# Kernel optimization log

Hardware: AMD Instinct MI355X
Metric: run time of the kernel (lower is better)

## Reference

```python
import jax, jax.numpy as jnp
import numpy as np
from jax.ops import segment_sum

N_NODES = 100000
IN_C, HID_C, OUT_C = 128, 128, 64
N_EDGES = 1600000


def gcn_conv(x, row, col, dinv, W, b):
    # PyG GCNConv: symmetric normalization with self-loops.
    # h = X W; out[c] = sum_{(r,c) in E} dinv[r]*dinv[c]*h[r] + dinv[v]^2*h[v] + b
    h = x @ W  # [N, F_out]
    norm = dinv[row] * dinv[col]  # [E]
    agg = segment_sum(h[row] * norm[:, None], col, num_segments=x.shape[0])
    agg = agg + h * (dinv * dinv)[:, None]  # self-loop contribution
    return agg + b


def setup_inputs() -> dict:
    key = jax.random.key(0)
    k1, k2, k3, k4, k5, k6 = jax.random.split(key, 6)
    x = jax.random.normal(k1, (N_NODES, IN_C), dtype=jnp.float32)
    edge_index = jax.random.randint(k2, (2, N_EDGES), 0, N_NODES, dtype=jnp.int64)
    # Glorot-style init for GCN weights, zero bias (as in PyG GCNConv)
    W1 = jax.random.normal(k3, (IN_C, HID_C), dtype=jnp.float32) / np.sqrt(IN_C)
    b1 = jnp.zeros((HID_C,), dtype=jnp.float32)
    W2 = jax.random.normal(k4, (HID_C, OUT_C), dtype=jnp.float32) / np.sqrt(HID_C)
    b2 = jnp.zeros((OUT_C,), dtype=jnp.float32)
    return {"x": x, "edge_index": edge_index, "W1": W1, "b1": b1, "W2": W2, "b2": b2}


def reference(x, edge_index, W1, b1, W2, b2):
    row, col = edge_index[0], edge_index[1]
    n = x.shape[0]
    # degree counts include self-loop (+1)
    deg = segment_sum(jnp.ones_like(col, dtype=x.dtype), col, num_segments=n) + 1.0
    dinv = jax.lax.rsqrt(deg)
    h = gcn_conv(x, row, col, dinv, W1, b1)
    h = jax.nn.relu(h)
    # dropout is identity in eval mode (get_embedding runs model.eval())
    out = gcn_conv(h, row, col, dinv, W2, b2)
    return out
```

## Files before the change

kernel.cpp:

```cpp
#include <hip/hip_runtime.h>
#include <math.h>


#define BS 256
#define EPB 4096
#define BK_SHIFT 9

typedef __attribute__((ext_vector_type(8))) short bf16x8;
typedef __attribute__((ext_vector_type(4))) float f32x4;
typedef __attribute__((ext_vector_type(4))) unsigned u32x4;

union FragU {
    bf16x8 v;
    unsigned u[4];
};

__device__ __forceinline__ unsigned pack_bf16x2(float a, float b) {
    unsigned ua = __float_as_uint(a);
    unsigned ub = __float_as_uint(b);
    ua = (ua + 0x7fffu + ((ua >> 16) & 1u)) >> 16;
    ub = (ub + 0x7fffu + ((ub >> 16) & 1u)) >> 16;
    return ua | (ub << 16);
}

__device__ __forceinline__ ushort bf16_rte(float a) {
    unsigned ua = __float_as_uint(a);
    return (ushort)((ua + 0x7fffu + ((ua >> 16) & 1u)) >> 16);
}

__device__ __forceinline__ float bf_lo(unsigned u) { return __uint_as_float(u << 16); }
__device__ __forceinline__ float bf_hi(unsigned u) { return __uint_as_float(u & 0xffff0000u); }

__global__ __launch_bounds__(BS) void p1_hist_kernel(const int* __restrict__ col,
                                                     int* __restrict__ countsT,
                                                     int E, int NBUCK, int NBLK) {
    __shared__ int h[256];
    int tid = threadIdx.x;
    h[tid] = 0;
    __syncthreads();
    int e0 = blockIdx.x * EPB;
    int e1 = min(e0 + EPB, E);
    for (int i = e0 + tid; i < e1; i += BS) atomicAdd(&h[col[i] >> BK_SHIFT], 1);
    __syncthreads();
    for (int b = tid; b < NBUCK; b += BS) countsT[b * NBLK + blockIdx.x] = h[b];
}

__global__ __launch_bounds__(BS) void scan_block_kernel(const int* __restrict__ in,
                                                        int* __restrict__ exc,
                                                        int* __restrict__ bsum, int N) {
    __shared__ int s[BS];
    int tid = threadIdx.x;
    int i = blockIdx.x * BS + tid;
    int v = (i < N) ? in[i] : 0;
    s[tid] = v;
    __syncthreads();
    for (int off = 1; off < BS; off <<= 1) {
        int t = (tid >= off) ? s[tid - off] : 0;
        __syncthreads();
        s[tid] += t;
        __syncthreads();
    }
    if (i < N) exc[i] = s[tid] - v;
    if (tid == BS - 1) bsum[blockIdx.x] = s[BS - 1];
}

__global__ __launch_bounds__(512) void scan_bsum_kernel(const int* __restrict__ bsum,
                                                        int* __restrict__ boff, int NB) {
    __shared__ int s[512];
    int tid = threadIdx.x;
    int v = (tid < NB) ? bsum[tid] : 0;
    s[tid] = v;
    __syncthreads();
    for (int off = 1; off < 512; off <<= 1) {
        int t = (tid >= off) ? s[tid - off] : 0;
        __syncthreads();
        s[tid] += t;
        __syncthreads();
    }
    if (tid < NB) boff[tid] = s[tid] - v;
}

__global__ __launch_bounds__(BS) void p2_scatter_kernel(const int* __restrict__ row,
                                                        const int* __restrict__ col,
                                                        const int* __restrict__ baseT,
                                                        const int* __restrict__ boff,
                                                        uint2* __restrict__ pairs,
                                                        int E, int NBUCK, int NBLK) {
    __shared__ int cur[256];
    int tid = threadIdx.x;
    for (int b = tid; b < NBUCK; b += BS) {
        int idx = b * NBLK + blockIdx.x;
        cur[b] = baseT[idx] + boff[idx >> 8];
    }
    __syncthreads();
    int e0 = blockIdx.x * EPB;
    int e1 = min(e0 + EPB, E);
    for (int i = e0 + tid; i < e1; i += BS) {
        int c = col[i];
        int r = row[i];
        int pos = atomicAdd(&cur[c >> BK_SHIFT], 1);
        pairs[pos] = make_uint2((unsigned)r, (unsigned)c);
    }
}

__global__ __launch_bounds__(BS) void p3_build_kernel(const uint2* __restrict__ pairs,
                                                      const int* __restrict__ baseT,
                                                      const int* __restrict__ boff,
                                                      int* __restrict__ off_g,
                                                      int* __restrict__ deg_g,
                                                      float* __restrict__ dinv,
                                                      int* __restrict__ src,
                                                      int E, int n, int NBUCK, int NBLK) {
    __shared__ int cnt[512];
    __shared__ int scn[512];
    __shared__ int a256[256];
    int tid = threadIdx.x;
    int b = blockIdx.x;
    int i0 = b * NBLK;
    int s = baseT[i0] + boff[i0 >> 8];
    int eEnd;
    if (b == NBUCK - 1) {
        eEnd = E;
    } else {
        int i1 = (b + 1) * NBLK;
        eEnd = baseT[i1] + boff[i1 >> 8];
    }

    cnt[tid] = 0;
    cnt[tid + 256] = 0;
    __syncthreads();
    for (int i = s + tid; i < eEnd; i += BS) {
        uint2 p = pairs[i];
        atomicAdd(&cnt[p.y & 511], 1);
    }
    __syncthreads();
    int pairsum = cnt[2 * tid] + cnt[2 * tid + 1];
    a256[tid] = pairsum;
    __syncthreads();
    for (int off = 1; off < 256; off <<= 1) {
        int t = (tid >= off) ? a256[tid - off] : 0;
        __syncthreads();
        a256[tid] += t;
        __syncthreads();
    }
    int exc = a256[tid] - pairsum;
    scn[2 * tid] = exc;
    scn[2 * tid + 1] = exc + cnt[2 * tid];
    __syncthreads();
#pragma unroll
    for (int l = tid; l < 512; l += BS) {
        int node = (b << BK_SHIFT) + l;
        if (node < n) {
            off_g[node] = s + scn[l];
            deg_g[node] = cnt[l];
            dinv[node] = rsqrtf((float)(cnt[l] + 1));
        }
    }
    __syncthreads();
#pragma unroll
    for (int l = tid; l < 512; l += BS) scn[l] += s;
    __syncthreads();
    for (int i = s + tid; i < eEnd; i += BS) {
        uint2 p = pairs[i];
        int pos = atomicAdd(&scn[p.y & 511], 1);
        src[pos] = (int)p.x;
    }
}

__global__ __launch_bounds__(BS) void wprep_kernel(const float* __restrict__ W1,
                                                   const float* __restrict__ W2,
                                                   ushort* __restrict__ wt1,
                                                   ushort* __restrict__ wt2) {
    int t = blockIdx.x * BS + threadIdx.x;
    if (t < 128 * 128) {
        int nn = t >> 7, k = t & 127;
        wt1[t] = bf16_rte(W1[k * 128 + nn]);
    }
    if (t < 64 * 128) {
        int nn = t >> 7, k = t & 127;
        wt2[t] = bf16_rte(W2[k * 64 + nn]);
    }
}

template <int NCH, bool IN_BF16>
__global__ __launch_bounds__(BS) void gemm_mfma_kernel(const void* __restrict__ Ain,
                                                       const ushort* __restrict__ WT,
                                                       const float* __restrict__ dinv,
                                                       unsigned* __restrict__ G, int n) {
    constexpr int NT = NCH / 16;
    constexpr int KP = 136;
    __shared__ ushort wlds[NCH * KP];

    int tid = threadIdx.x;
    for (int c = tid; c < NCH * 16; c += BS) {
        int nr = c >> 4, q16 = c & 15;
        *(uint4*)(wlds + nr * KP + q16 * 8) = ((const uint4*)WT)[c];
    }
    __syncthreads();

    int lane = tid & 63, wv = tid >> 6;
    int ml = lane & 15, quad = lane >> 4;
    int m = blockIdx.x * 64 + wv * 16 + ml;

    FragU b[4];
    if (m < n) {
        if (IN_BF16) {
#pragma unroll
            for (int ks = 0; ks < 4; ++ks) {
                uint4 t = ((const uint4*)Ain)[(size_t)m * 16 + ks * 4 + quad];
                b[ks].u[0] = t.x; b[ks].u[1] = t.y; b[ks].u[2] = t.z; b[ks].u[3] = t.w;
            }
        } else {
            const float4* A = (const float4*)Ain + (size_t)m * 32;
#pragma unroll
            for (int ks = 0; ks < 4; ++ks) {
                float4 p0 = A[ks * 8 + quad * 2];
                float4 p1 = A[ks * 8 + quad * 2 + 1];
                b[ks].u[0] = pack_bf16x2(p0.x, p0.y);
                b[ks].u[1] = pack_bf16x2(p0.z, p0.w);
                b[ks].u[2] = pack_bf16x2(p1.x, p1.y);
                b[ks].u[3] = pack_bf16x2(p1.z, p1.w);
            }
        }
    } else {
#pragma unroll
        for (int ks = 0; ks < 4; ++ks) {
            b[ks].u[0] = 0; b[ks].u[1] = 0; b[ks].u[2] = 0; b[ks].u[3] = 0;
        }
    }

    f32x4 acc[NT];
#pragma unroll
    for (int nt = 0; nt < NT; ++nt) {
        acc[nt][0] = 0.f; acc[nt][1] = 0.f; acc[nt][2] = 0.f; acc[nt][3] = 0.f;
    }

#pragma unroll
    for (int nt = 0; nt < NT; ++nt) {
#pragma unroll
        for (int ks = 0; ks < 4; ++ks) {
            bf16x8 a = *(const bf16x8*)(wlds + (nt * 16 + ml) * KP + ks * 32 + quad * 8);
            acc[nt] = __builtin_amdgcn_mfma_f32_16x16x32_bf16(a, b[ks].v, acc[nt], 0, 0, 0);
        }
    }

    if (m < n) {
        float dv = dinv[m];
        unsigned* grow = G + (size_t)m * (NCH / 2);
#pragma unroll
        for (int nt = 0; nt < NT; ++nt) {
            uint2 o;
            o.x = pack_bf16x2(acc[nt][0] * dv, acc[nt][1] * dv);
            o.y = pack_bf16x2(acc[nt][2] * dv, acc[nt][3] * dv);
            *(uint2*)(grow + nt * 8 + quad * 2) = o;
        }
    }
}

template <int C, bool RELU, bool OUT_BF16>
__global__ __launch_bounds__(BS) void agg_kernel(const unsigned* __restrict__ G,
                                                 const int* __restrict__ edge_off,
                                                 const int* __restrict__ cnt,
                                                 const int* __restrict__ src,
                                                 const float* __restrict__ dinv,
                                                 const float* __restrict__ bias,
                                                 void* __restrict__ out, int n) {
    constexpr int Gp = C / 8;
    constexpr int NPB = BS / Gp;
    int lane = threadIdx.x & (Gp - 1);
    int li = threadIdx.x / Gp;
    int node = blockIdx.x * NPB + li;
    if (node >= n) return;

    const uint4* G4 = (const uint4*)G;
    float acc[8];
    {
        uint4 sv = G4[(size_t)node * Gp + lane];
        acc[0] = bf_lo(sv.x); acc[1] = bf_hi(sv.x);
        acc[2] = bf_lo(sv.y); acc[3] = bf_hi(sv.y);
        acc[4] = bf_lo(sv.z); acc[5] = bf_hi(sv.z);
        acc[6] = bf_lo(sv.w); acc[7] = bf_hi(sv.w);
    }
    const int* sp = src + edge_off[node];
    int deg = cnt[node];

#define ACCUM(v)                                                               \
    acc[0] += bf_lo(v.x); acc[1] += bf_hi(v.x);                                \
    acc[2] += bf_lo(v.y); acc[3] += bf_hi(v.y);                                \
    acc[4] += bf_lo(v.z); acc[5] += bf_hi(v.z);                                \
    acc[6] += bf_lo(v.w); acc[7] += bf_hi(v.w);

    if constexpr (Gp == 16) {
        int i = 0;
        for (; i + Gp <= deg; i += Gp) {
            int myi = __builtin_nontemporal_load(sp + i + lane);
#pragma unroll
            for (int h = 0; h < Gp / 8; ++h) {
                uint4 v[8];
#pragma unroll
                for (int u = 0; u < 8; ++u) {
                    int s = __shfl(myi, h * 8 + u, Gp);
                    v[u] = G4[(size_t)s * Gp + lane];
                }
#pragma unroll
                for (int u = 0; u < 8; ++u) { ACCUM(v[u]) }
            }
        }
        int rem = deg - i;
        if (rem > 0) {
            int myi = (lane < rem) ? __builtin_nontemporal_load(sp + i + lane) : 0;
            int j = 0;
            if (rem >= 8) {
                uint4 v[8];
#pragma unroll
                for (int u = 0; u < 8; ++u) {
                    int s = __shfl(myi, u, Gp);
                    v[u] = G4[(size_t)s * Gp + lane];
                }
#pragma unroll
                for (int u = 0; u < 8; ++u) { ACCUM(v[u]) }
                j = 8;
            }
            if (rem - j >= 4) {
                uint4 v[4];
#pragma unroll
                for (int u = 0; u < 4; ++u) {
                    int s = __shfl(myi, j + u, Gp);
                    v[u] = G4[(size_t)s * Gp + lane];
                }
#pragma unroll
                for (int u = 0; u < 4; ++u) { ACCUM(v[u]) }
                j += 4;
            }
            if (rem - j >= 2) {
                int s0 = __shfl(myi, j, Gp);
                int s1 = __shfl(myi, j + 1, Gp);
                uint4 v0 = G4[(size_t)s0 * Gp + lane];
                uint4 v1 = G4[(size_t)s1 * Gp + lane];
                ACCUM(v0) ACCUM(v1)
                j += 2;
            }
            if (rem - j >= 1) {
                int s0 = __shfl(myi, j, Gp);
                uint4 v0 = G4[(size_t)s0 * Gp + lane];
                ACCUM(v0)
            }
        }
    } else {
        int myi0 = __builtin_nontemporal_load(sp + lane);
        int myi1 = __builtin_nontemporal_load(sp + 8 + lane);
        int i = 0;
        for (; i + 16 <= deg; i += 16) {
            int nx0 = __builtin_nontemporal_load(sp + i + 16 + lane);
            int nx1 = __builtin_nontemporal_load(sp + i + 24 + lane);
            uint4 v[8];
#pragma unroll
            for (int u = 0; u < 8; ++u) {
                int s = __shfl(myi0, u, Gp);
                v[u] = G4[(size_t)s * Gp + lane];
            }
#pragma unroll
            for (int u = 0; u < 8; ++u) { ACCUM(v[u]) }
#pragma unroll
            for (int u = 0; u < 8; ++u) {
                int s = __shfl(myi1, u, Gp);
                v[u] = G4[(size_t)s * Gp + lane];
            }
#pragma unroll
            for (int u = 0; u < 8; ++u) { ACCUM(v[u]) }
            myi0 = nx0;
            myi1 = nx1;
        }
        int rem = deg - i;
        if (rem >= 8) {
            uint4 v[8];
#pragma unroll
            for (int u = 0; u < 8; ++u) {
                int s = __shfl(myi0, u, Gp);
                v[u] = G4[(size_t)s * Gp + lane];
            }
#pragma unroll
            for (int u = 0; u < 8; ++u) { ACCUM(v[u]) }
        }
        int rest = (rem >= 8) ? myi1 : myi0;
        int jb = 0;
        int r2 = rem & 7;
        if (r2 >= 4) {
            uint4 v[4];
#pragma unroll
            for (int u = 0; u < 4; ++u) {
                int s = __shfl(rest, jb + u, Gp);
                v[u] = G4[(size_t)s * Gp + lane];
            }
#pragma unroll
            for (int u = 0; u < 4; ++u) { ACCUM(v[u]) }
            jb += 4;
        }
        if (r2 & 2) {
            int s0 = __shfl(rest, jb, Gp);
            int s1 = __shfl(rest, jb + 1, Gp);
            uint4 v0 = G4[(size_t)s0 * Gp + lane];
            uint4 v1 = G4[(size_t)s1 * Gp + lane];
            ACCUM(v0) ACCUM(v1)
            jb += 2;
        }
        if (r2 & 1) {
            int s0 = __shfl(rest, jb, Gp);
            uint4 v0 = G4[(size_t)s0 * Gp + lane];
            ACCUM(v0)
        }
    }
#undef ACCUM

    float dv = dinv[node];
    const float4* b4 = (const float4*)bias;
    float4 bl = b4[2 * lane + 0], bh = b4[2 * lane + 1];
    float o0x = acc[0] * dv + bl.x, o0y = acc[1] * dv + bl.y;
    float o0z = acc[2] * dv + bl.z, o0w = acc[3] * dv + bl.w;
    float o1x = acc[4] * dv + bh.x, o1y = acc[5] * dv + bh.y;
    float o1z = acc[6] * dv + bh.z, o1w = acc[7] * dv + bh.w;
    if (RELU) {
        o0x = fmaxf(o0x, 0.f); o0y = fmaxf(o0y, 0.f);
        o0z = fmaxf(o0z, 0.f); o0w = fmaxf(o0w, 0.f);
        o1x = fmaxf(o1x, 0.f); o1y = fmaxf(o1y, 0.f);
        o1z = fmaxf(o1z, 0.f); o1w = fmaxf(o1w, 0.f);
    }
    if (OUT_BF16) {
        u32x4 ov;
        ov.x = pack_bf16x2(o0x, o0y);
        ov.y = pack_bf16x2(o0z, o0w);
        ov.z = pack_bf16x2(o1x, o1y);
        ov.w = pack_bf16x2(o1z, o1w);
        __builtin_nontemporal_store(ov, (u32x4*)out + (size_t)node * Gp + lane);
    } else {
        f32x4* orow = (f32x4*)((float*)out + (size_t)node * C);
        f32x4 o0; o0.x = o0x; o0.y = o0y; o0.z = o0z; o0.w = o0w;
        f32x4 o1; o1.x = o1x; o1.y = o1y; o1.z = o1z; o1.w = o1w;
        __builtin_nontemporal_store(o0, orow + 2 * lane + 0);
        __builtin_nontemporal_store(o1, orow + 2 * lane + 1);
    }
}

extern "C" void kernel_launch(void* const* d_in, const int* in_sizes, int n_in,
                              void* d_out, int out_size, void* d_ws, size_t ws_size,
                              hipStream_t stream) {
    const float* x  = (const float*)d_in[0];
    const int*   ei = (const int*)d_in[1];
    const float* W1 = (const float*)d_in[2];
    const float* b1 = (const float*)d_in[3];
    const float* W2 = (const float*)d_in[4];
    const float* b2 = (const float*)d_in[5];

    const int IN_C = 128, HID_C = 128;
    int n = in_sizes[0] / IN_C;
    int E = in_sizes[1] / 2;
    const int* row = ei;
    const int* col = ei + E;

    int NBUCK = (n + 511) >> BK_SHIFT;
    int NBLK = (E + EPB - 1) / EPB;
    int M = NBUCK * NBLK;
    int NBS = (M + BS - 1) / BS;

    char* w = (char*)d_ws;
    auto alloc = [&](size_t bytes) {
        void* p = (void*)w;
        w += (bytes + 255) & ~(size_t)255;
        return p;
    };
    int*      countsT = (int*)alloc((size_t)M * 4);
    int*      baseT   = (int*)alloc((size_t)M * 4);
    int*      bsum    = (int*)alloc((size_t)NBS * 4);
    int*      boff    = (int*)alloc((size_t)NBS * 4);
    uint2*    pairs   = (uint2*)alloc((size_t)E * 8);
    int*      src     = (int*)alloc((size_t)E * 4);
    int*      off     = (int*)alloc((size_t)n * 4);
    int*      deg     = (int*)alloc((size_t)n * 4);
    float*    dinv    = (float*)alloc((size_t)n * 4);
    ushort*   wt1     = (ushort*)alloc(128 * 128 * 2);
    ushort*   wt2     = (ushort*)alloc(64 * 128 * 2);
    unsigned* g       = (unsigned*)alloc((size_t)n * HID_C * 2);
    unsigned* h1b     = (unsigned*)alloc((size_t)n * HID_C * 2);

    wprep_kernel<<<64, BS, 0, stream>>>(W1, W2, wt1, wt2);

    p1_hist_kernel<<<NBLK, BS, 0, stream>>>(col, countsT, E, NBUCK, NBLK);
    scan_block_kernel<<<NBS, BS, 0, stream>>>(countsT, baseT, bsum, M);
    scan_bsum_kernel<<<1, 512, 0, stream>>>(bsum, boff, NBS);
    p2_scatter_kernel<<<NBLK, BS, 0, stream>>>(row, col, baseT, boff, pairs,
                                               E, NBUCK, NBLK);
    p3_build_kernel<<<NBUCK, BS, 0, stream>>>(pairs, baseT, boff, off, deg, dinv,
                                              src, E, n, NBUCK, NBLK);

    int gridM = (n + 63) / 64;

    gemm_mfma_kernel<128, false><<<gridM, BS, 0, stream>>>(x, wt1, dinv, g, n);
    agg_kernel<128, true, true><<<(n + 15) / 16, BS, 0, stream>>>(g, off, deg, src,
                                                                  dinv, b1, h1b, n);

    gemm_mfma_kernel<64, true><<<gridM, BS, 0, stream>>>(h1b, wt2, dinv, g, n);
    agg_kernel<64, false, false><<<(n + 31) / 32, BS, 0, stream>>>(g, off, deg, src,
                                                                   dinv, b2, d_out, n);
}
```

Before: 276.7 us.

## Replace two-pass bucket sort CSR build with global atomic counting sort

Replaces the bucketed histogram, scatter-to-pairs and per-bucket local sort with a direct counting sort: global atomic degree counts, a prefix scan over nodes, and a placement pass using global atomics on per-node cursors. This drops the intermediate pairs buffer and one extra pass over all edges. In exchange it relies on contended global atomics with random addresses and writes src in scattered order. Edge order within a node becomes nondeterministic, which can change float summation order.

```diff
diff --git a/kernel.cpp b/kernel.cpp
--- a/kernel.cpp
+++ b/kernel.cpp
@@ -3,8 +3,6 @@
 
 
 #define BS 256
-#define EPB 4096
-#define BK_SHIFT 9
 
 typedef __attribute__((ext_vector_type(8))) short bf16x8;
 typedef __attribute__((ext_vector_type(4))) float f32x4;
@@ -31,18 +29,38 @@
 __device__ __forceinline__ float bf_lo(unsigned u) { return __uint_as_float(u << 16); }
 __device__ __forceinline__ float bf_hi(unsigned u) { return __uint_as_float(u & 0xffff0000u); }
 
-__global__ __launch_bounds__(BS) void p1_hist_kernel(const int* __restrict__ col,
-                                                     int* __restrict__ countsT,
-                                                     int E, int NBUCK, int NBLK) {
-    __shared__ int h[256];
-    int tid = threadIdx.x;
-    h[tid] = 0;
-    __syncthreads();
-    int e0 = blockIdx.x * EPB;
-    int e1 = min(e0 + EPB, E);
-    for (int i = e0 + tid; i < e1; i += BS) atomicAdd(&h[col[i] >> BK_SHIFT], 1);
-    __syncthreads();
-    for (int b = tid; b < NBUCK; b += BS) countsT[b * NBLK + blockIdx.x] = h[b];
+__global__ __launch_bounds__(BS) void wprep_zero_kernel(const float* __restrict__ W1,
+                                                        const float* __restrict__ W2,
+                                                        ushort* __restrict__ wt1,
+                                                        ushort* __restrict__ wt2,
+                                                        int* __restrict__ deg, int n) {
+    int t = blockIdx.x * BS + threadIdx.x;
+    int NT = gridDim.x * BS;
+    for (int i = t; i < n; i += NT) deg[i] = 0;
+    if (t < 128 * 128) {
+        int nn = t >> 7, k = t & 127;
+        wt1[t] = bf16_rte(W1[k * 128 + nn]);
+    }
+    if (t < 64 * 128) {
+        int nn = t >> 7, k = t & 127;
+        wt2[t] = bf16_rte(W2[k * 64 + nn]);
+    }
+}
+
+__global__ __launch_bounds__(BS) void count_kernel(const int* __restrict__ col,
+                                                   int* __restrict__ deg, int E) {
+    int t = blockIdx.x * BS + threadIdx.x;
+    int n4 = E >> 2;
+    const int4* c4 = (const int4*)col;
+    if (t < n4) {
+        int4 c = c4[t];
+        atomicAdd(&deg[c.x], 1);
+        atomicAdd(&deg[c.y], 1);
+        atomicAdd(&deg[c.z], 1);
+        atomicAdd(&deg[c.w], 1);
+    }
+    int r = (n4 << 2) + t;
+    if (r < E) atomicAdd(&deg[col[r]], 1);
 }
 
 __global__ __launch_bounds__(BS) void scan_block_kernel(const int* __restrict__ in,
@@ -80,105 +98,45 @@
     if (tid < NB) boff[tid] = s[tid] - v;
 }
 
-__global__ __launch_bounds__(BS) void p2_scatter_kernel(const int* __restrict__ row,
-                                                        const int* __restrict__ col,
-                                                        const int* __restrict__ baseT,
-                                                        const int* __restrict__ boff,
-                                                        uint2* __restrict__ pairs,
-                                                        int E, int NBUCK, int NBLK) {
-    __shared__ int cur[256];
-    int tid = threadIdx.x;
-    for (int b = tid; b < NBUCK; b += BS) {
-        int idx = b * NBLK + blockIdx.x;
-        cur[b] = baseT[idx] + boff[idx >> 8];
-    }
-    __syncthreads();
-    int e0 = blockIdx.x * EPB;
-    int e1 = min(e0 + EPB, E);
-    for (int i = e0 + tid; i < e1; i += BS) {
-        int c = col[i];
-        int r = row[i];
-        int pos = atomicAdd(&cur[c >> BK_SHIFT], 1);
-        pairs[pos] = make_uint2((unsigned)r, (unsigned)c);
-    }
-}
-
-__global__ __launch_bounds__(BS) void p3_build_kernel(const uint2* __restrict__ pairs,
-                                                      const int* __restrict__ baseT,
-                                                      const int* __restrict__ boff,
-                                                      int* __restrict__ off_g,
-                                                      int* __restrict__ deg_g,
-                                                      float* __restrict__ dinv,
-                                                      int* __restrict__ src,
-                                                      int E, int n, int NBUCK, int NBLK) {
-    __shared__ int cnt[512];
-    __shared__ int scn[512];
-    __shared__ int a256[256];
-    int tid = threadIdx.x;
-    int b = blockIdx.x;
-    int i0 = b * NBLK;
-    int s = baseT[i0] + boff[i0 >> 8];
-    int eEnd;
-    if (b == NBUCK - 1) {
-        eEnd = E;
-    } else {
-        int i1 = (b + 1) * NBLK;
-        eEnd = baseT[i1] + boff[i1 >> 8];
-    }
-
-    cnt[tid] = 0;
-    cnt[tid + 256] = 0;
-    __syncthreads();
-    for (int i = s + tid; i < eEnd; i += BS) {
-        uint2 p = pairs[i];
-        atomicAdd(&cnt[p.y & 511], 1);
-    }
-    __syncthreads();
-    int pairsum = cnt[2 * tid] + cnt[2 * tid + 1];
-    a256[tid] = pairsum;
-    __syncthreads();
-    for (int off = 1; off < 256; off <<= 1) {
-        int t = (tid >= off) ? a256[tid - off] : 0;
-        __syncthreads();
-        a256[tid] += t;
-        __syncthreads();
-    }
-    int exc = a256[tid] - pairsum;
-    scn[2 * tid] = exc;
-    scn[2 * tid + 1] = exc + cnt[2 * tid];
-    __syncthreads();
-#pragma unroll
-    for (int l = tid; l < 512; l += BS) {
-        int node = (b << BK_SHIFT) + l;
-        if (node < n) {
-            off_g[node] = s + scn[l];
-            deg_g[node] = cnt[l];
-            dinv[node] = rsqrtf((float)(cnt[l] + 1));
-        }
-    }
-    __syncthreads();
-#pragma unroll
-    for (int l = tid; l < 512; l += BS) scn[l] += s;
-    __syncthreads();
-    for (int i = s + tid; i < eEnd; i += BS) {
-        uint2 p = pairs[i];
-        int pos = atomicAdd(&scn[p.y & 511], 1);
-        src[pos] = (int)p.x;
-    }
-}
-
-__global__ __launch_bounds__(BS) void wprep_kernel(const float* __restrict__ W1,
-                                                   const float* __restrict__ W2,
-                                                   ushort* __restrict__ wt1,
-                                                   ushort* __restrict__ wt2) {
+__global__ __launch_bounds__(BS) void init_kernel(const int* __restrict__ exc,
+                                                  const int* __restrict__ boff,
+                                                  const int* __restrict__ deg,
+                                                  int* __restrict__ off,
+                                                  int* __restrict__ cur,
+                                                  float* __restrict__ dinv, int n) {
+    int i = blockIdx.x * BS + threadIdx.x;
+    if (i < n) {
+        int base = exc[i] + boff[i >> 8];
+        off[i] = base;
+        cur[i] = base;
+        dinv[i] = rsqrtf((float)(deg[i] + 1));
+    }
+}
+
+__global__ __launch_bounds__(BS) void place_kernel(const int* __restrict__ row,
+                                                   const int* __restrict__ col,
+                                                   int* __restrict__ cur,
+                                                   int* __restrict__ src, int E) {
     int t = blockIdx.x * BS + threadIdx.x;
-    if (t < 128 * 128) {
-        int nn = t >> 7, k = t & 127;
-        wt1[t] = bf16_rte(W1[k * 128 + nn]);
-    }
-    if (t < 64 * 128) {
-        int nn = t >> 7, k = t & 127;
-        wt2[t] = bf16_rte(W2[k * 64 + nn]);
+    int n4 = E >> 2;
+    const int4* c4 = (const int4*)col;
+    const int4* r4 = (const int4*)row;
+    if (t < n4) {
+        int4 c = c4[t];
+        int4 r = r4[t];
+        int p0 = atomicAdd(&cur[c.x], 1);
+        int p1 = atomicAdd(&cur[c.y], 1);
+        int p2 = atomicAdd(&cur[c.z], 1);
+        int p3 = atomicAdd(&cur[c.w], 1);
+        src[p0] = r.x;
+        src[p1] = r.y;
+        src[p2] = r.z;
+        src[p3] = r.w;
+    }
+    int rr = (n4 << 2) + t;
+    if (rr < E) {
+        int p = atomicAdd(&cur[col[rr]], 1);
+        src[p] = row[rr];
     }
 }
 
@@ -457,10 +415,7 @@
     const int* row = ei;
     const int* col = ei + E;
 
-    int NBUCK = (n + 511) >> BK_SHIFT;
-    int NBLK = (E + EPB - 1) / EPB;
-    int M = NBUCK * NBLK;
-    int NBS = (M + BS - 1) / BS;
+    int NBS = (n + BS - 1) / BS;
 
     char* w = (char*)d_ws;
     auto alloc = [&](size_t bytes) {
@@ -468,29 +423,29 @@
         w += (bytes + 255) & ~(size_t)255;
         return p;
     };
-    int*      countsT = (int*)alloc((size_t)M * 4);
-    int*      baseT   = (int*)alloc((size_t)M * 4);
+    int*      deg     = (int*)alloc((size_t)n * 4);
+    int*      exc     = (int*)alloc((size_t)n * 4);
     int*      bsum    = (int*)alloc((size_t)NBS * 4);
     int*      boff    = (int*)alloc((size_t)NBS * 4);
-    uint2*    pairs   = (uint2*)alloc((size_t)E * 8);
+    int*      cur     = (int*)alloc((size_t)n * 4);
+    int*      off     = (int*)alloc((size_t)n * 4);
+    float*    dinv    = (float*)alloc((size_t)n * 4);
     int*      src     = (int*)alloc((size_t)E * 4);
-    int*      off     = (int*)alloc((size_t)n * 4);
-    int*      deg     = (int*)alloc((size_t)n * 4);
-    float*    dinv    = (float*)alloc((size_t)n * 4);
     ushort*   wt1     = (ushort*)alloc(128 * 128 * 2);
     ushort*   wt2     = (ushort*)alloc(64 * 128 * 2);
     unsigned* g       = (unsigned*)alloc((size_t)n * HID_C * 2);
     unsigned* h1b     = (unsigned*)alloc((size_t)n * HID_C * 2);
 
-    wprep_kernel<<<64, BS, 0, stream>>>(W1, W2, wt1, wt2);
-
-    p1_hist_kernel<<<NBLK, BS, 0, stream>>>(col, countsT, E, NBUCK, NBLK);
-    scan_block_kernel<<<NBS, BS, 0, stream>>>(countsT, baseT, bsum, M);
+    int n4 = E >> 2;
+    int gridE = (n4 + BS - 1) / BS;
+
+    wprep_zero_kernel<<<64, BS, 0, stream>>>(W1, W2, wt1, wt2, deg, n);
+
+    count_kernel<<<gridE, BS, 0, stream>>>(col, deg, E);
+    scan_block_kernel<<<NBS, BS, 0, stream>>>(deg, exc, bsum, n);
     scan_bsum_kernel<<<1, 512, 0, stream>>>(bsum, boff, NBS);
-    p2_scatter_kernel<<<NBLK, BS, 0, stream>>>(row, col, baseT, boff, pairs,
-                                               E, NBUCK, NBLK);
-    p3_build_kernel<<<NBUCK, BS, 0, stream>>>(pairs, baseT, boff, off, deg, dinv,
-                                              src, E, n, NBUCK, NBLK);
+    init_kernel<<<NBS, BS, 0, stream>>>(exc, boff, deg, off, cur, dinv, n);
+    place_kernel<<<gridE, BS, 0, stream>>>(row, col, cur, src, E);
 
     int gridM = (n + 63) / 64;
 
```

After: 412.0 us. +48.9%, slower.

## Fuse CSR build stages into one cooperative kernel with grid syncs

Applied to the files above, without the earlier changes.

Merges weight prep, histogram, two-level scan, scatter and per-bucket CSR build into a single cooperative launch of 256 blocks separated by grid.sync(), replacing six kernel launches. It also drops the edges-per-block count from 4096 (about 391 blocks) to 256 blocks of about 6250 edges each, which shrinks the count matrix. The goal is to remove launch gaps and tail effects between the small preprocessing kernels. In exchange, grid-wide barriers cost something, only 256 blocks run the edge passes, and the build phase still uses only NBUCK (about 196) blocks.

```diff
diff --git a/kernel.cpp b/kernel.cpp
--- a/kernel.cpp
+++ b/kernel.cpp
@@ -1,10 +1,13 @@
 #include <hip/hip_runtime.h>
+#include <hip/hip_cooperative_groups.h>
 #include <math.h>
 
 
 #define BS 256
-#define EPB 4096
 #define BK_SHIFT 9
+#define NG 256
+
+namespace cg = cooperative_groups;
 
 typedef __attribute__((ext_vector_type(8))) short bf16x8;
 typedef __attribute__((ext_vector_type(4))) float f32x4;
@@ -31,154 +34,140 @@
 __device__ __forceinline__ float bf_lo(unsigned u) { return __uint_as_float(u << 16); }
 __device__ __forceinline__ float bf_hi(unsigned u) { return __uint_as_float(u & 0xffff0000u); }
 
-__global__ __launch_bounds__(BS) void p1_hist_kernel(const int* __restrict__ col,
-                                                     int* __restrict__ countsT,
-                                                     int E, int NBUCK, int NBLK) {
-    __shared__ int h[256];
+__global__ __launch_bounds__(BS) void csr_fused_kernel(
+        const int* __restrict__ row, const int* __restrict__ col,
+        const float* __restrict__ W1, const float* __restrict__ W2,
+        ushort* __restrict__ wt1, ushort* __restrict__ wt2,
+        int* __restrict__ countsT, int* __restrict__ bsum,
+        int* __restrict__ boff, uint2* __restrict__ pairs,
+        int* __restrict__ off_g, int* __restrict__ deg_g,
+        float* __restrict__ dinv, int* __restrict__ src,
+        int E, int n, int NBUCK, int NSC) {
+    cg::grid_group grid = cg::this_grid();
+    __shared__ int s1[512];
+    __shared__ int s2[512];
+    __shared__ int s3[256];
+
     int tid = threadIdx.x;
-    h[tid] = 0;
+    int blk = blockIdx.x;
+    int gt = blk * BS + tid;
+    int M = NBUCK * NG;
+    int EPB = (E + NG - 1) / NG;
+    int e0 = blk * EPB;
+    int e1 = min(e0 + EPB, E);
+
+    if (gt < 128 * 128) {
+        int nn = gt >> 7, k = gt & 127;
+        wt1[gt] = bf16_rte(W1[k * 128 + nn]);
+    }
+    if (gt < 64 * 128) {
+        int nn = gt >> 7, k = gt & 127;
+        wt2[gt] = bf16_rte(W2[k * 64 + nn]);
+    }
+    s3[tid] = 0;
     __syncthreads();
-    int e0 = blockIdx.x * EPB;
-    int e1 = min(e0 + EPB, E);
-    for (int i = e0 + tid; i < e1; i += BS) atomicAdd(&h[col[i] >> BK_SHIFT], 1);
+    for (int i = e0 + tid; i < e1; i += BS) atomicAdd(&s3[col[i] >> BK_SHIFT], 1);
     __syncthreads();
-    for (int b = tid; b < NBUCK; b += BS) countsT[b * NBLK + blockIdx.x] = h[b];
-}
-
-__global__ __launch_bounds__(BS) void scan_block_kernel(const int* __restrict__ in,
-                                                        int* __restrict__ exc,
-                                                        int* __restrict__ bsum, int N) {
-    __shared__ int s[BS];
-    int tid = threadIdx.x;
-    int i = blockIdx.x * BS + tid;
-    int v = (i < N) ? in[i] : 0;
-    s[tid] = v;
+    for (int b = tid; b < NBUCK; b += BS) countsT[b * NG + blk] = s3[b];
+    grid.sync();
+
+    if (blk < NSC) {
+        int i = blk * BS + tid;
+        int v = (i < M) ? countsT[i] : 0;
+        s3[tid] = v;
+        __syncthreads();
+        for (int off = 1; off < BS; off <<= 1) {
+            int t = (tid >= off) ? s3[tid - off] : 0;
+            __syncthreads();
+            s3[tid] += t;
+            __syncthreads();
+        }
+        if (i < M) countsT[i] = s3[tid] - v;
+        if (tid == BS - 1) bsum[blk] = s3[BS - 1];
+    }
+    grid.sync();
+
+    if (blk == 0) {
+        int carry = 0;
+        for (int c0 = 0; c0 < NSC; c0 += BS) {
+            int idx = c0 + tid;
+            int v = (idx < NSC) ? bsum[idx] : 0;
+            s3[tid] = v;
+            __syncthreads();
+            for (int off = 1; off < BS; off <<= 1) {
+                int t = (tid >= off) ? s3[tid - off] : 0;
+                __syncthreads();
+                s3[tid] += t;
+                __syncthreads();
+            }
+            if (idx < NSC) boff[idx] = s3[tid] - v + carry;
+            int tot = s3[BS - 1];
+            __syncthreads();
+            carry += tot;
+        }
+    }
+    grid.sync();
+
+    if (blk < NSC) {
+        int i = blk * BS + tid;
+        if (i < M) countsT[i] += boff[blk];
+    }
+    grid.sync();
+
+    for (int b = tid; b < NBUCK; b += BS) s3[b] = countsT[b * NG + blk];
     __syncthreads();
-    for (int off = 1; off < BS; off <<= 1) {
-        int t = (tid >= off) ? s[tid - off] : 0;
-        __syncthreads();
-        s[tid] += t;
-        __syncthreads();
-    }
-    if (i < N) exc[i] = s[tid] - v;
-    if (tid == BS - 1) bsum[blockIdx.x] = s[BS - 1];
-}
-
-__global__ __launch_bounds__(512) void scan_bsum_kernel(const int* __restrict__ bsum,
-                                                        int* __restrict__ boff, int NB) {
-    __shared__ int s[512];
-    int tid = threadIdx.x;
-    int v = (tid < NB) ? bsum[tid] : 0;
-    s[tid] = v;
-    __syncthreads();
-    for (int off = 1; off < 512; off <<= 1) {
-        int t = (tid >= off) ? s[tid - off] : 0;
-        __syncthreads();
-        s[tid] += t;
-        __syncthreads();
-    }
-    if (tid < NB) boff[tid] = s[tid] - v;
-}
-
-__global__ __launch_bounds__(BS) void p2_scatter_kernel(const int* __restrict__ row,
-                                                        const int* __restrict__ col,
-                                                        const int* __restrict__ baseT,
-                                                        const int* __restrict__ boff,
-                                                        uint2* __restrict__ pairs,
-                                                        int E, int NBUCK, int NBLK) {
-    __shared__ int cur[256];
-    int tid = threadIdx.x;
-    for (int b = tid; b < NBUCK; b += BS) {
-        int idx = b * NBLK + blockIdx.x;
-        cur[b] = baseT[idx] + boff[idx >> 8];
-    }
-    __syncthreads();
-    int e0 = blockIdx.x * EPB;
-    int e1 = min(e0 + EPB, E);
     for (int i = e0 + tid; i < e1; i += BS) {
         int c = col[i];
         int r = row[i];
-        int pos = atomicAdd(&cur[c >> BK_SHIFT], 1);
+        int pos = atomicAdd(&s3[c >> BK_SHIFT], 1);
         pairs[pos] = make_uint2((unsigned)r, (unsigned)c);
     }
-}
-
-__global__ __launch_bounds__(BS) void p3_build_kernel(const uint2* __restrict__ pairs,
-                                                      const int* __restrict__ baseT,
-                                                      const int* __restrict__ boff,
-                                                      int* __restrict__ off_g,
-                                                      int* __restrict__ deg_g,
-                                                      float* __restrict__ dinv,
-                                                      int* __restrict__ src,
-                                                      int E, int n, int NBUCK, int NBLK) {
-    __shared__ int cnt[512];
-    __shared__ int scn[512];
-    __shared__ int a256[256];
-    int tid = threadIdx.x;
-    int b = blockIdx.x;
-    int i0 = b * NBLK;
-    int s = baseT[i0] + boff[i0 >> 8];
-    int eEnd;
-    if (b == NBUCK - 1) {
-        eEnd = E;
-    } else {
-        int i1 = (b + 1) * NBLK;
-        eEnd = baseT[i1] + boff[i1 >> 8];
-    }
-
-    cnt[tid] = 0;
-    cnt[tid + 256] = 0;
-    __syncthreads();
-    for (int i = s + tid; i < eEnd; i += BS) {
-        uint2 p = pairs[i];
-        atomicAdd(&cnt[p.y & 511], 1);
-    }
-    __syncthreads();
-    int pairsum = cnt[2 * tid] + cnt[2 * tid + 1];
-    a256[tid] = pairsum;
-    __syncthreads();
-    for (int off = 1; off < 256; off <<= 1) {
-        int t = (tid >= off) ? a256[tid - off] : 0;
-        __syncthreads();
-        a256[tid] += t;
-        __syncthreads();
-    }
-    int exc = a256[tid] - pairsum;
-    scn[2 * tid] = exc;
-    scn[2 * tid + 1] = exc + cnt[2 * tid];
-    __syncthreads();
-#pragma unroll
-    for (int l = tid; l < 512; l += BS) {
-        int node = (b << BK_SHIFT) + l;
-        if (node < n) {
-            off_g[node] = s + scn[l];
-            deg_g[node] = cnt[l];
-            dinv[node] = rsqrtf((float)(cnt[l] + 1));
-        }
-    }
-    __syncthreads();
-#pragma unroll
-    for (int l = tid; l < 512; l += BS) scn[l] += s;
-    __syncthreads();
-    for (int i = s + tid; i < eEnd; i += BS) {
-        uint2 p = pairs[i];
-        int pos = atomicAdd(&scn[p.y & 511], 1);
-        src[pos] = (int)p.x;
-    }
-}
-
-__global__ __launch_bounds__(BS) void wprep_kernel(const float* __restrict__ W1,
-                                                   const float* __restrict__ W2,
-                                                   ushort* __restrict__ wt1,
-                                                   ushort* __restrict__ wt2) {
-    int t = blockIdx.x * BS + threadIdx.x;
-    if (t < 128 * 128) {
-        int nn = t >> 7, k = t & 127;
-        wt1[t] = bf16_rte(W1[k * 128 + nn]);
-    }
-    if (t < 64 * 128) {
-        int nn = t >> 7, k = t & 127;
-        wt2[t] = bf16_rte(W2[k * 64 + nn]);
+    grid.sync();
+
+    if (blk < NBUCK) {
+        int b = blk;
+        int s = countsT[b * NG];
+        int eEnd = (b == NBUCK - 1) ? E : countsT[(b + 1) * NG];
+
+        s1[tid] = 0;
+        s1[tid + 256] = 0;
+        __syncthreads();
+        for (int i = s + tid; i < eEnd; i += BS) {
+            uint2 p = pairs[i];
+            atomicAdd(&s1[p.y & 511], 1);
+        }
+        __syncthreads();
+        int pairsum = s1[2 * tid] + s1[2 * tid + 1];
+        s3[tid] = pairsum;
+        __syncthreads();
+        for (int off = 1; off < 256; off <<= 1) {
+            int t = (tid >= off) ? s3[tid - off] : 0;
+            __syncthreads();
+            s3[tid] += t;
+            __syncthreads();
+        }
+        int exc = s3[tid] - pairsum;
+        s2[2 * tid] = exc;
+        s2[2 * tid + 1] = exc + s1[2 * tid];
+        __syncthreads();
+#pragma unroll
+        for (int l = tid; l < 512; l += BS) {
+            int node = (b << BK_SHIFT) + l;
+            if (node < n) {
+                off_g[node] = s + s2[l];
+                deg_g[node] = s1[l];
+                dinv[node] = rsqrtf((float)(s1[l] + 1));
+            }
+        }
+        __syncthreads();
+#pragma unroll
+        for (int l = tid; l < 512; l += BS) s2[l] += s;
+        __syncthreads();
+        for (int i = s + tid; i < eEnd; i += BS) {
+            uint2 p = pairs[i];
+            int pos = atomicAdd(&s2[p.y & 511], 1);
+            src[pos] = (int)p.x;
+        }
     }
 }
 
@@ -458,9 +447,8 @@
     const int* col = ei + E;
 
     int NBUCK = (n + 511) >> BK_SHIFT;
-    int NBLK = (E + EPB - 1) / EPB;
-    int M = NBUCK * NBLK;
-    int NBS = (M + BS - 1) / BS;
+    int M = NBUCK * NG;
+    int NSC = (M + BS - 1) / BS;
 
     char* w = (char*)d_ws;
     auto alloc = [&](size_t bytes) {
@@ -469,9 +457,8 @@
         return p;
     };
     int*      countsT = (int*)alloc((size_t)M * 4);
-    int*      baseT   = (int*)alloc((size_t)M * 4);
-    int*      bsum    = (int*)alloc((size_t)NBS * 4);
-    int*      boff    = (int*)alloc((size_t)NBS * 4);
+    int*      bsum    = (int*)alloc((size_t)NSC * 4);
+    int*      boff    = (int*)alloc((size_t)NSC * 4);
     uint2*    pairs   = (uint2*)alloc((size_t)E * 8);
     int*      src     = (int*)alloc((size_t)E * 4);
     int*      off     = (int*)alloc((size_t)n * 4);
@@ -482,15 +469,15 @@
     unsigned* g       = (unsigned*)alloc((size_t)n * HID_C * 2);
     unsigned* h1b     = (unsigned*)alloc((size_t)n * HID_C * 2);
 
-    wprep_kernel<<<64, BS, 0, stream>>>(W1, W2, wt1, wt2);
-
-    p1_hist_kernel<<<NBLK, BS, 0, stream>>>(col, countsT, E, NBUCK, NBLK);
-    scan_block_kernel<<<NBS, BS, 0, stream>>>(countsT, baseT, bsum, M);
-    scan_bsum_kernel<<<1, 512, 0, stream>>>(bsum, boff, NBS);
-    p2_scatter_kernel<<<NBLK, BS, 0, stream>>>(row, col, baseT, boff, pairs,
-                                               E, NBUCK, NBLK);
-    p3_build_kernel<<<NBUCK, BS, 0, stream>>>(pairs, baseT, boff, off, deg, dinv,
-                                              src, E, n, NBUCK, NBLK);
+    void* kargs[] = {
+        (void*)&row, (void*)&col, (void*)&W1, (void*)&W2,
+        (void*)&wt1, (void*)&wt2, (void*)&countsT, (void*)&bsum,
+        (void*)&boff, (void*)&pairs, (void*)&off, (void*)&deg,
+        (void*)&dinv, (void*)&src, (void*)&E, (void*)&n,
+        (void*)&NBUCK, (void*)&NSC,
+    };
+    hipLaunchCooperativeKernel((void*)csr_fused_kernel, dim3(NG), dim3(BS),
+                               kargs, 0, stream);
 
     int gridM = (n + 63) / 64;
 
```

Measured after the change: 428.3 us. 1.55x slower.
